# Kernel optimization log

Measured on AMD Instinct MI355X. Metric: run time of the kernel, lower is better.

## Reference

```python
import jax, jax.numpy as jnp
import numpy as np
import math

B = 512
EMB = 512
CLASSNUM = 70722
M = 0.4
H = 0.333
S = 64.0
EPS = 1e-3


def setup_inputs() -> dict:
    key = jax.random.key(0)
    k1, k2, k3, k4, k5 = jax.random.split(key, 5)
    embbedings = jax.random.normal(k1, (B, EMB), dtype=jnp.float32)
    # feature norms: positive, realistic range ~[1, 30)
    norms = jax.random.uniform(k2, (B, 1), dtype=jnp.float32) * 29.0 + 1.0
    label = jax.random.randint(k3, (B,), 0, CLASSNUM, dtype=jnp.int64)
    class_sample_num_ = jax.random.uniform(k4, (B,), dtype=jnp.float32) * 9.0 + 1.0
    kernel = jax.random.normal(k5, (EMB, CLASSNUM), dtype=jnp.float32)
    return {
        "embbedings": embbedings,
        "norms": norms,
        "label": label,
        "class_sample_num_": class_sample_num_,
        "kernel": kernel,
    }


def reference(embbedings, norms, label, class_sample_num_, kernel):
    # l2-normalize kernel columns (axis=0)
    kernel_norm = kernel / jnp.linalg.norm(kernel, axis=0, keepdims=True)
    cosine = jnp.matmul(embbedings, kernel_norm)  # [B, C]
    cosine = jnp.clip(cosine, -1.0 + EPS, 1.0 - EPS)

    # detached margin scaler path (torch uses .detach / no_grad)
    safe_norms = jnp.clip(norms, 0.001, 100.0)
    safe_norms = safe_norms / (class_sample_num_[:, None] + 0.001)
    safe_norms = jnp.clip(safe_norms, 0.001, 100.0)
    safe_norms = jax.lax.stop_gradient(safe_norms)

    mean = jnp.mean(safe_norms)
    std = jnp.std(safe_norms, ddof=1)  # torch.std is unbiased
    # t_alpha = 1.0 => batch stats are exactly this batch's mean/std
    batch_mean, batch_std = mean, std

    margin_scaler = (safe_norms - batch_mean) / (batch_std + EPS)
    margin_scaler = jnp.clip(margin_scaler * H, -1.0, 1.0)  # [B, 1]
    ms = margin_scaler[:, 0]  # [B]

    rows = jnp.arange(B)
    lab = label.astype(jnp.int32)

    # angular margin: theta_m = clip(theta + onehot * (-m*ms))
    theta = jnp.arccos(cosine)
    theta = theta.at[rows, lab].add(-M * ms)
    theta_m = jnp.clip(theta, EPS, math.pi - EPS)
    cosine2 = jnp.cos(theta_m)

    # additive margin at the label column: g_add = m + m*ms
    cosine2 = cosine2.at[rows, lab].add(-(M + M * ms))

    return cosine2 * S
```

## Files before the change

### kernel.cpp

```cpp
#include <hip/hip_runtime.h>
#include <math.h>

#define CLASSNUM 70722
#define BATCH 512
#define EMBD 512
#define M_C 0.4f
#define H_C 0.333f
#define S_C 64.0f
#define EPS_C 0.001f
#define PI_F 3.14159265358979f

typedef __bf16 bf16_t;
typedef __bf16 bf16x8 __attribute__((ext_vector_type(8)));
typedef float f32x4 __attribute__((ext_vector_type(4)));

__device__ __forceinline__ float clampf(float x, float lo, float hi) {
    return fminf(fmaxf(x, lo), hi);
}

__global__ __launch_bounds__(256) void prep_lab_kernel(
    const float* __restrict__ emb, const float* __restrict__ norms,
    const float* __restrict__ csn, const int* __restrict__ label,
    const float* __restrict__ kmat, bf16_t* __restrict__ Aws,
    float* __restrict__ labout)
{
    __shared__ float red[256];
    const int tid = threadIdx.x;
    const int bi = blockIdx.x;

    if (bi < 128) {
        const int G = bi * 256 + tid;
        const int kt = G >> 11;
        const int rem = G & 2047;
        const int rg = rem >> 6;
        const int lane = rem & 63;
        const int row = rg * 16 + (lane & 15);
        const int k0 = kt * 32 + (lane >> 4) * 8;
        const float* src = emb + row * EMBD + k0;
        const float4 v0 = *(const float4*)src;
        const float4 v1 = *(const float4*)(src + 4);
        bf16x8 bw;
        bw[0] = (bf16_t)v0.x; bw[1] = (bf16_t)v0.y;
        bw[2] = (bf16_t)v0.z; bw[3] = (bf16_t)v0.w;
        bw[4] = (bf16_t)v1.x; bw[5] = (bf16_t)v1.y;
        bw[6] = (bf16_t)v1.z; bw[7] = (bf16_t)v1.w;
        *(bf16x8*)(Aws + (size_t)G * 8) = bw;
        return;
    }

    const int b = bi - 128;

    float s0, s1;
    {
        float sn = clampf(norms[tid], 0.001f, 100.0f);
        sn = sn / (csn[tid] + 0.001f);
        s0 = clampf(sn, 0.001f, 100.0f);
    }
    {
        float sn = clampf(norms[tid + 256], 0.001f, 100.0f);
        sn = sn / (csn[tid + 256] + 0.001f);
        s1 = clampf(sn, 0.001f, 100.0f);
    }
    red[tid] = s0 + s1;
    __syncthreads();
    for (int off = 128; off > 0; off >>= 1) {
        if (tid < off) red[tid] += red[tid + off];
        __syncthreads();
    }
    const float mean = red[0] * (1.0f / 512.0f);
    __syncthreads();
    const float d0 = s0 - mean, d1 = s1 - mean;
    red[tid] = d0 * d0 + d1 * d1;
    __syncthreads();
    for (int off = 128; off > 0; off >>= 1) {
        if (tid < off) red[tid] += red[tid + off];
        __syncthreads();
    }
    const float stdv = sqrtf(red[0] * (1.0f / 511.0f));
    __syncthreads();

    const int lab = label[b];
    const float* col = kmat + lab;
    const float* e = emb + b * EMBD;
    float dot = 0.0f, ss = 0.0f;
#pragma unroll
    for (int k = tid; k < EMBD; k += 256) {
        const float kv = col[(size_t)k * CLASSNUM];
        const float ev = e[k];
        dot = fmaf(ev, kv, dot);
        ss  = fmaf(kv, kv, ss);
    }
    red[tid] = dot;
    __syncthreads();
    for (int off = 128; off > 0; off >>= 1) {
        if (tid < off) red[tid] += red[tid + off];
        __syncthreads();
    }
    const float dotT = red[0];
    __syncthreads();
    red[tid] = ss;
    __syncthreads();
    for (int off = 128; off > 0; off >>= 1) {
        if (tid < off) red[tid] += red[tid + off];
        __syncthreads();
    }
    if (tid == 0) {
        const float ssT = red[0];
        float c = dotT / sqrtf(ssT);
        c = clampf(c, -1.0f + EPS_C, 1.0f - EPS_C);
        float snb = clampf(norms[b], 0.001f, 100.0f);
        snb = snb / (csn[b] + 0.001f);
        snb = clampf(snb, 0.001f, 100.0f);
        const float msv = clampf((snb - mean) / (stdv + EPS_C) * H_C, -1.0f, 1.0f);
        float th = acosf(c) - M_C * msv;
        th = clampf(th, EPS_C, PI_F - EPS_C);
        labout[b] = (cosf(th) - (M_C + M_C * msv)) * S_C;
    }
}


#define LOADB(kt, bv) do {                                              \
    const size_t kb_ = (size_t)((kt) * 32) * CLASSNUM;                  \
    _Pragma("unroll")                                                   \
    for (int ni_ = 0; ni_ < 4; ++ni_) {                                 \
        _Pragma("unroll")                                               \
        for (int j_ = 0; j_ < 8; ++j_)                                  \
            bv[ni_][j_] = bq[ni_][kb_ + (size_t)j_ * CLASSNUM];         \
    }                                                                   \
} while (0)

#define LOADA(kt, af) do {                                              \
    const bf16x8* ap_ = (const bf16x8*)Aws                              \
        + (((kt) * 32 + wave * 4) * 64 + lane);                         \
    _Pragma("unroll")                                                   \
    for (int mi_ = 0; mi_ < 4; ++mi_) af[mi_] = ap_[mi_ * 64];          \
} while (0)

#define CVTB(bv, bfr) do {                                              \
    _Pragma("unroll")                                                   \
    for (int ni_ = 0; ni_ < 4; ++ni_) {                                 \
        _Pragma("unroll")                                               \
        for (int j_ = 0; j_ < 8; ++j_) {                                \
            const float v_ = bv[ni_][j_];                               \
            ssq[ni_] = fmaf(v_, v_, ssq[ni_]);                          \
            bfr[ni_][j_] = (bf16_t)v_;                                  \
        }                                                               \
    }                                                                   \
} while (0)

#define DOMFMA(af, bfr) do {                                            \
    _Pragma("unroll")                                                   \
    for (int mi_ = 0; mi_ < 4; ++mi_) {                                 \
        _Pragma("unroll")                                               \
        for (int ni_ = 0; ni_ < 4; ++ni_)                               \
            acc[mi_][ni_] = __builtin_amdgcn_mfma_f32_16x16x32_bf16(    \
                af[mi_], bfr[ni_], acc[mi_][ni_], 0, 0, 0);             \
    }                                                                   \
} while (0)

__global__ __launch_bounds__(512, 2) void gemm_kernel(
    const bf16_t* __restrict__ Aws, const float* __restrict__ Kmat,
    const int* __restrict__ label, const float* __restrict__ labout,
    float* __restrict__ out)
{
    __shared__ int   lab_s[BATCH];
    __shared__ float lo_s[BATCH];
    const int tid = threadIdx.x;
    lab_s[tid] = label[tid];
    lo_s[tid]  = labout[tid];
    __syncthreads();

    const int lane = tid & 63;
    const int wave = tid >> 6;
    const int r16  = lane & 15;
    const int quad = lane >> 4;
    const int n0   = blockIdx.x * 64;

    const float* bq[4];
    bool cok[4];
#pragma unroll
    for (int ni = 0; ni < 4; ++ni) {
        int c = n0 + ni * 16 + r16;
        cok[ni] = (c < CLASSNUM);
        c = cok[ni] ? c : (CLASSNUM - 1);
        bq[ni] = Kmat + (size_t)(quad * 8) * CLASSNUM + c;
    }

    f32x4 acc[4][4];
    const f32x4 zero = {0.0f, 0.0f, 0.0f, 0.0f};
#pragma unroll
    for (int i = 0; i < 4; ++i)
#pragma unroll
        for (int j = 0; j < 4; ++j) acc[i][j] = zero;
    float ssq[4] = {0.0f, 0.0f, 0.0f, 0.0f};

    float bvA[4][8], bvB[4][8];
    bf16x8 afC[4], afN[4];

    LOADB(0, bvA);
    LOADB(1, bvB);
    LOADA(0, afC);

#pragma unroll 1
    for (int p = 0; p < 7; ++p) {
        {
            bf16x8 bfr[4];
            CVTB(bvA, bfr);
            LOADB(2 * p + 2, bvA);
            LOADA(2 * p + 1, afN);
            DOMFMA(afC, bfr);
        }
        {
            bf16x8 bfr[4];
            CVTB(bvB, bfr);
            LOADB(2 * p + 3, bvB);
            LOADA(2 * p + 2, afC);
            DOMFMA(afN, bfr);
        }
    }
    {
        bf16x8 bfr[4];
        CVTB(bvA, bfr);
        LOADA(15, afN);
        DOMFMA(afC, bfr);
    }
    {
        bf16x8 bfr[4];
        CVTB(bvB, bfr);
        DOMFMA(afN, bfr);
    }

    float invn[4];
#pragma unroll
    for (int ni = 0; ni < 4; ++ni) {
        float s = ssq[ni];
        s += __shfl_xor(s, 16);
        s += __shfl_xor(s, 32);
        invn[ni] = (s > 0.0f) ? (1.0f / sqrtf(s)) : 0.0f;
    }

#pragma unroll
    for (int mi = 0; mi < 4; ++mi) {
#pragma unroll
        for (int rr = 0; rr < 4; ++rr) {
            const int row = wave * 64 + mi * 16 + quad * 4 + rr;
            const int labc = lab_s[row];
            const float lov = lo_s[row];
            float* orow = out + (size_t)row * CLASSNUM;
#pragma unroll
            for (int ni = 0; ni < 4; ++ni) {
                if (cok[ni]) {
                    const int col = n0 + ni * 16 + r16;
                    const float c = clampf(acc[mi][ni][rr] * invn[ni],
                                           -1.0f + EPS_C, 1.0f - EPS_C);
                    float v = c * S_C;
                    if (labc == col) v = lov;
                    orow[col] = v;
                }
            }
        }
    }
}

extern "C" void kernel_launch(void* const* d_in, const int* in_sizes, int n_in,
                              void* d_out, int out_size, void* d_ws, size_t ws_size,
                              hipStream_t stream)
{
    const float* emb   = (const float*)d_in[0];
    const float* norms = (const float*)d_in[1];
    const int*   label = (const int*)d_in[2];
    const float* csn   = (const float*)d_in[3];
    const float* kmat  = (const float*)d_in[4];
    float* out = (float*)d_out;

    const size_t A_BYTES = (size_t)BATCH * EMBD * sizeof(bf16_t);
    if (ws_size < A_BYTES + 4096) return;
    bf16_t* Aws   = (bf16_t*)d_ws;
    float* labout = (float*)((char*)d_ws + A_BYTES);

    prep_lab_kernel<<<128 + BATCH, 256, 0, stream>>>(
        emb, norms, csn, label, kmat, Aws, labout);
    const int nblk = (CLASSNUM + 63) / 64;
    gemm_kernel<<<nblk, 512, 0, stream>>>(Aws, kmat, label, labout, out);
}
```

Measured before the change: 382.8 us.

## Stage kernel tiles through LDS so each K element is loaded once per block

Previously every wave loaded the full 64-column by 512-row fp32 kernel tile itself, so each element was fetched eight times per block. Now each thread loads a 4-row slice, converts it to bf16 into a double-buffered LDS tile, and all waves read MFMA operands from LDS. Column-norm partial sums are reduced through shared memory, and block indices are remapped so contiguous column ranges land on the same XCD. Launch bounds rise to 4 blocks per SM. The cost is a barrier every K step and extra LDS traffic.

```diff
diff --git a/kernel.cpp b/kernel.cpp
--- a/kernel.cpp
+++ b/kernel.cpp
@@ -11,6 +11,7 @@
 #define PI_F 3.14159265358979f
 
 typedef __bf16 bf16_t;
+typedef __bf16 bf16x4 __attribute__((ext_vector_type(4)));
 typedef __bf16 bf16x8 __attribute__((ext_vector_type(8)));
 typedef float f32x4 __attribute__((ext_vector_type(4)));
 
@@ -119,72 +120,83 @@
 }
 
 
-#define LOADB(kt, bv) do {                                              \
-    const size_t kb_ = (size_t)((kt) * 32) * CLASSNUM;                  \
-    _Pragma("unroll")                                                   \
-    for (int ni_ = 0; ni_ < 4; ++ni_) {                                 \
-        _Pragma("unroll")                                               \
-        for (int j_ = 0; j_ < 8; ++j_)                                  \
-            bv[ni_][j_] = bq[ni_][kb_ + (size_t)j_ * CLASSNUM];         \
+#define LOADB4(t, dst) do {                                             \
+    const size_t ko_ = (size_t)((t) * 32) * CLASSNUM;                   \
+    _Pragma("unroll")                                                   \
+    for (int j_ = 0; j_ < 4; ++j_)                                      \
+        dst[j_] = bp[ko_ + (size_t)j_ * CLASSNUM];                      \
+} while (0)
+
+#define LOADA4(t, af) do {                                              \
+    const bf16x8* ap_ = (const bf16x8*)Aws                              \
+        + (((t) * 32 + wave * 4) * 64 + lane);                          \
+    _Pragma("unroll")                                                   \
+    for (int mi_ = 0; mi_ < 4; ++mi_) af[mi_] = ap_[mi_ * 64];          \
+} while (0)
+
+#define CVTW(src, buf) do {                                             \
+    bf16x4 w_;                                                          \
+    _Pragma("unroll")                                                   \
+    for (int j_ = 0; j_ < 4; ++j_) {                                    \
+        const float v_ = src[j_];                                       \
+        ssq = fmaf(v_, v_, ssq);                                        \
+        w_[j_] = (bf16_t)v_;                                            \
     }                                                                   \
-} while (0)
-
-#define LOADA(kt, af) do {                                              \
-    const bf16x8* ap_ = (const bf16x8*)Aws                              \
-        + (((kt) * 32 + wave * 4) * 64 + lane);                         \
-    _Pragma("unroll")                                                   \
-    for (int mi_ = 0; mi_ < 4; ++mi_) af[mi_] = ap_[mi_ * 64];          \
-} while (0)
-
-#define CVTB(bv, bfr) do {                                              \
-    _Pragma("unroll")                                                   \
-    for (int ni_ = 0; ni_ < 4; ++ni_) {                                 \
-        _Pragma("unroll")                                               \
-        for (int j_ = 0; j_ < 8; ++j_) {                                \
-            const float v_ = bv[ni_][j_];                               \
-            ssq[ni_] = fmaf(v_, v_, ssq[ni_]);                          \
-            bfr[ni_][j_] = (bf16_t)v_;                                  \
-        }                                                               \
-    }                                                                   \
-} while (0)
-
-#define DOMFMA(af, bfr) do {                                            \
-    _Pragma("unroll")                                                   \
-    for (int mi_ = 0; mi_ < 4; ++mi_) {                                 \
+    *(bf16x4*)&Blds[buf][c * 40 + kg * 4] = w_;                         \
+} while (0)
+
+#define MFMA16(af, buf) do {                                            \
+    bf16x8 bfr_[4];                                                     \
+    _Pragma("unroll")                                                   \
+    for (int ni_ = 0; ni_ < 4; ++ni_)                                   \
+        bfr_[ni_] = *(const bf16x8*)                                    \
+            &Blds[buf][(ni_ * 16 + r16) * 40 + quad * 8];               \
+    _Pragma("unroll")                                                   \
+    for (int mi_ = 0; mi_ < 4; ++mi_)                                   \
         _Pragma("unroll")                                               \
         for (int ni_ = 0; ni_ < 4; ++ni_)                               \
             acc[mi_][ni_] = __builtin_amdgcn_mfma_f32_16x16x32_bf16(    \
-                af[mi_], bfr[ni_], acc[mi_][ni_], 0, 0, 0);             \
-    }                                                                   \
-} while (0)
-
-__global__ __launch_bounds__(512, 2) void gemm_kernel(
+                af[mi_], bfr_[ni_], acc[mi_][ni_], 0, 0, 0);            \
+} while (0)
+
+#define BARRIER() do {                                                  \
+    asm volatile("s_waitcnt lgkmcnt(0)" ::: "memory");                  \
+    __builtin_amdgcn_s_barrier();                                       \
+} while (0)
+
+__global__ __launch_bounds__(512, 4) void gemm_kernel(
     const bf16_t* __restrict__ Aws, const float* __restrict__ Kmat,
     const int* __restrict__ label, const float* __restrict__ labout,
     float* __restrict__ out)
 {
+    __shared__ bf16_t Blds[2][64 * 40];
+    __shared__ float red[512];
+    __shared__ float invn_s[64];
     __shared__ int   lab_s[BATCH];
     __shared__ float lo_s[BATCH];
-    const int tid = threadIdx.x;
-    lab_s[tid] = label[tid];
-    lo_s[tid]  = labout[tid];
-    __syncthreads();
-
+
+    const int tid  = threadIdx.x;
     const int lane = tid & 63;
     const int wave = tid >> 6;
     const int r16  = lane & 15;
     const int quad = lane >> 4;
-    const int n0   = blockIdx.x * 64;
-
-    const float* bq[4];
-    bool cok[4];
-#pragma unroll
-    for (int ni = 0; ni < 4; ++ni) {
-        int c = n0 + ni * 16 + r16;
-        cok[ni] = (c < CLASSNUM);
-        c = cok[ni] ? c : (CLASSNUM - 1);
-        bq[ni] = Kmat + (size_t)(quad * 8) * CLASSNUM + c;
-    }
+
+    const int nwg = (CLASSNUM + 63) / 64;
+    const int q_ = nwg >> 3, r_ = nwg & 7;
+    const int xcd = blockIdx.x & 7, idx = blockIdx.x >> 3;
+    const int nb = (xcd < r_) ? (xcd * (q_ + 1) + idx)
+                              : (r_ * (q_ + 1) + (xcd - r_) * q_ + idx);
+    const int n0 = nb * 64;
+
+    lab_s[tid] = label[tid];
+    lo_s[tid]  = labout[tid];
+
+    const int c  = tid & 63;
+    const int kg = tid >> 6;
+    int cg = n0 + c;
+    const bool cv = (cg < CLASSNUM);
+    if (!cv) cg = CLASSNUM - 1;
+    const float* bp = Kmat + (size_t)(kg * 4) * CLASSNUM + cg;
 
     f32x4 acc[4][4];
     const f32x4 zero = {0.0f, 0.0f, 0.0f, 0.0f};
@@ -192,52 +204,44 @@
     for (int i = 0; i < 4; ++i)
 #pragma unroll
         for (int j = 0; j < 4; ++j) acc[i][j] = zero;
-    float ssq[4] = {0.0f, 0.0f, 0.0f, 0.0f};
-
-    float bvA[4][8], bvB[4][8];
-    bf16x8 afC[4], afN[4];
-
-    LOADB(0, bvA);
-    LOADB(1, bvB);
-    LOADA(0, afC);
+    float ssq = 0.0f;
+
+    float bv0[4], bv1[4];
+
+    LOADB4(0, bv0);
+    LOADB4(1, bv1);
+    CVTW(bv0, 0);
+    BARRIER();
 
 #pragma unroll 1
-    for (int p = 0; p < 7; ++p) {
+    for (int p = 0; p < 8; ++p) {
         {
-            bf16x8 bfr[4];
-            CVTB(bvA, bfr);
-            LOADB(2 * p + 2, bvA);
-            LOADA(2 * p + 1, afN);
-            DOMFMA(afC, bfr);
+            bf16x8 af[4];
+            LOADA4(2 * p, af);
+            if (p < 7) LOADB4(2 * p + 2, bv0);
+            MFMA16(af, 0);
+            CVTW(bv1, 1);
+            BARRIER();
         }
         {
-            bf16x8 bfr[4];
-            CVTB(bvB, bfr);
-            LOADB(2 * p + 3, bvB);
-            LOADA(2 * p + 2, afC);
-            DOMFMA(afN, bfr);
+            bf16x8 af[4];
+            LOADA4(2 * p + 1, af);
+            if (p < 7) LOADB4(2 * p + 3, bv1);
+            MFMA16(af, 1);
+            if (p < 7) CVTW(bv0, 0);
+            BARRIER();
         }
     }
-    {
-        bf16x8 bfr[4];
-        CVTB(bvA, bfr);
-        LOADA(15, afN);
-        DOMFMA(afC, bfr);
-    }
-    {
-        bf16x8 bfr[4];
-        CVTB(bvB, bfr);
-        DOMFMA(afN, bfr);
-    }
-
-    float invn[4];
-#pragma unroll
-    for (int ni = 0; ni < 4; ++ni) {
-        float s = ssq[ni];
-        s += __shfl_xor(s, 16);
-        s += __shfl_xor(s, 32);
-        invn[ni] = (s > 0.0f) ? (1.0f / sqrtf(s)) : 0.0f;
-    }
+
+    red[tid] = ssq;
+    __syncthreads();
+    if (tid < 64) {
+        float s = 0.0f;
+#pragma unroll
+        for (int g = 0; g < 8; ++g) s += red[tid + g * 64];
+        invn_s[tid] = (s > 0.0f) ? (1.0f / sqrtf(s)) : 0.0f;
+    }
+    __syncthreads();
 
 #pragma unroll
     for (int mi = 0; mi < 4; ++mi) {
@@ -249,11 +253,12 @@
             float* orow = out + (size_t)row * CLASSNUM;
 #pragma unroll
             for (int ni = 0; ni < 4; ++ni) {
-                if (cok[ni]) {
-                    const int col = n0 + ni * 16 + r16;
-                    const float c = clampf(acc[mi][ni][rr] * invn[ni],
-                                           -1.0f + EPS_C, 1.0f - EPS_C);
-                    float v = c * S_C;
+                const int col_loc = ni * 16 + r16;
+                const int col = n0 + col_loc;
+                if (col < CLASSNUM) {
+                    const float cc = clampf(acc[mi][ni][rr] * invn_s[col_loc],
+                                            -1.0f + EPS_C, 1.0f - EPS_C);
+                    float v = cc * S_C;
                     if (labc == col) v = lov;
                     orow[col] = v;
                 }
```

New measurement: 317.0 us. 17.2% less time.
